# Optimization experiments

Measured on AMD Instinct MI355X. Metric: run time of the kernel, lower is better.

## Reference

```python
import jax, jax.numpy as jnp
import numpy as np

B, C, H, W = 16, 512, 64, 64
CB, CG = 64, 256  # bottleneck = C/8, g = C/2


def _conv1x1(x, w, b):
    # x: [B,Cin,H,W], w: [Cout,Cin] -> [B,Cout,H,W]
    return jnp.einsum('bchw,oc->bohw', x, w) + b[None, :, None, None]


def _avg_pool2(x):
    # 2x2 average pool, stride 2. x: [B,C,H,W] with even H,W.
    b, c, h, w = x.shape
    return x.reshape(b, c, h // 2, 2, w // 2, 2).mean(axis=(3, 5))


def setup_inputs() -> dict:
    key = jax.random.key(0)
    ks = jax.random.split(key, 6)
    s = 0.02
    return {
        'x': jax.random.normal(ks[0], (B, C, H, W), jnp.float32),
        'w_theta': jax.random.normal(ks[1], (CB, C), jnp.float32) * s,
        'b_theta': jnp.zeros((CB,), jnp.float32),
        'w_phi': jax.random.normal(ks[2], (CB, C), jnp.float32) * s,
        'b_phi': jnp.zeros((CB,), jnp.float32),
        'w_g': jax.random.normal(ks[3], (CG, C), jnp.float32) * s,
        'b_g': jnp.zeros((CG,), jnp.float32),
        'w_out': jax.random.normal(ks[4], (C, CG), jnp.float32) * s,
        'b_out': jnp.zeros((C,), jnp.float32),
        'gamma': jnp.zeros((1,), jnp.float32),
    }


def reference(x, w_theta, b_theta, w_phi, b_phi, w_g, b_g, w_out, b_out, gamma):
    b, c, h, w = x.shape
    n = h * w          # query locations
    m = n // 4         # pooled key/value locations

    theta = _conv1x1(x, w_theta, b_theta).reshape(b, CB, n)           # [B,CB,N]
    phi = _avg_pool2(_conv1x1(x, w_phi, b_phi)).reshape(b, CB, m)     # [B,CB,M]
    g = _avg_pool2(_conv1x1(x, w_g, b_g)).reshape(b, CG, m)           # [B,CG,M]

    logits = jnp.einsum('bcn,bcm->bnm', theta, phi)                   # [B,N,M]
    attn = jax.nn.softmax(logits, axis=-1)
    out = jnp.einsum('bcm,bnm->bcn', g, attn).reshape(b, CG, h, w)    # [B,CG,H,W]
    out = _conv1x1(out, w_out, b_out)                                 # [B,C,H,W]
    return gamma[0] * out + x
```

## Files before the change

### kernel.cpp

```cpp
#include <hip/hip_runtime.h>
#include <math.h>


typedef unsigned short u16;
typedef short bf16x8 __attribute__((ext_vector_type(8)));
typedef float f32x16 __attribute__((ext_vector_type(16)));
typedef u16 u16x4 __attribute__((ext_vector_type(4)));
typedef int i32x4 __attribute__((ext_vector_type(4)));

#define MFMA32 __builtin_amdgcn_mfma_f32_32x32x16_bf16
#define B_ 16
#define C_ 512
#define N_ 4096
#define M_ 1024
#define LOG2E 1.44269504088896f
#define FIXMAX 8.0f

__device__ __forceinline__ u16 f2b(float f) {
  unsigned u = __float_as_uint(f);
  return (u16)((u + 0x7FFFu + ((u >> 16) & 1u)) >> 16);
}
__device__ __forceinline__ unsigned cvtpk(float a, float b) {
  unsigned r;
  asm("v_cvt_pk_bf16_f32 %0, %1, %2" : "=v"(r) : "v"(a), "v"(b));
  return r;
}
__device__ __forceinline__ void permswap(unsigned &a, unsigned &b) {
  asm("v_permlane32_swap_b32 %0, %1" : "+v"(a), "+v"(b));
}
__device__ __forceinline__ float exp2v(float a) {
  float r;
  asm("v_exp_f32 %0, %1" : "=v"(r) : "v"(a));
  return r;
}
__device__ __forceinline__ void async_cp16(u16* lds, const u16* g) {
  __builtin_amdgcn_global_load_lds(
      (const __attribute__((address_space(1))) unsigned int*)g,
      (__attribute__((address_space(3))) unsigned int*)lds, 16, 0, 0);
}
__device__ __forceinline__ f32x16 fz16() {
  f32x16 z;
#pragma unroll
  for (int i = 0; i < 16; ++i) z[i] = 0.0f;
  return z;
}


__global__ __launch_bounds__(256) void cvt_all_kernel(
    const float* __restrict__ w_theta, const float* __restrict__ w_phi,
    const float* __restrict__ w_g, const float* __restrict__ w_out,
    const float* __restrict__ gamma, u16* __restrict__ dth, u16* __restrict__ dph,
    u16* __restrict__ dg, u16* __restrict__ dwo) {
  int i = blockIdx.x * 256 + threadIdx.x;
  if (i < 16384) {
    const float* s = (i < 8192) ? w_theta : w_phi;
    u16* d = (i < 8192) ? dth : dph;
    float scale = (i < 8192) ? LOG2E : 1.0f;
    int j = i & 8191;
    int o = j >> 7, c = (j & 127) * 4;
    float4 vv = *(const float4*)(s + (size_t)o * 512 + c);
    int idx = (((o >> 5) * 8 + (c >> 6)) * 4 + ((c >> 4) & 3)) * 512 +
              (((c >> 3) & 1) * 32 + (o & 31)) * 8 + (c & 7);
    u16x4 ot = {f2b(vv.x * scale), f2b(vv.y * scale), f2b(vv.z * scale), f2b(vv.w * scale)};
    *(u16x4*)(d + idx) = ot;
  } else if (i < 49152) {
    int j = i - 16384;
    int o = j >> 7, c = (j & 127) * 4;
    float4 vv = *(const float4*)(w_g + (size_t)o * 512 + c);
    int idx = (((o >> 5) * 8 + (c >> 6)) * 4 + ((c >> 4) & 3)) * 512 +
              (((c >> 3) & 1) * 32 + (o & 31)) * 8 + (c & 7);
    u16x4 ot = {f2b(vv.x), f2b(vv.y), f2b(vv.z), f2b(vv.w)};
    *(u16x4*)(dg + idx) = ot;
  } else {
    int j = i - 49152;
    int o = j >> 6, k = (j & 63) * 4;
    float scale = gamma[0];
    float4 vv = *(const float4*)(w_out + (size_t)o * 256 + k);
    int idx = ((o >> 5) * 16 + (k >> 4)) * 512 +
              (((k >> 3) & 1) * 32 + (o & 31)) * 8 + (k & 7);
    u16x4 ot = {f2b(vv.x * scale), f2b(vv.y * scale), f2b(vv.z * scale), f2b(vv.w * scale)};
    *(u16x4*)(dwo + idx) = ot;
  }
}

__global__ __launch_bounds__(512) void prep_kernel(
    const float* __restrict__ x, const u16* __restrict__ wth,
    const u16* __restrict__ wph, const u16* __restrict__ wg,
    const float* __restrict__ bth, const float* __restrict__ bph,
    const float* __restrict__ bg, u16* __restrict__ th, u16* __restrict__ ph,
    u16* __restrict__ vt) {
  __shared__ u16 xb[128 * 68];
  __shared__ u16 xpt[32 * 68];
  const int t = threadIdx.x;
  const int w = t >> 6, l = t & 63, lo = l & 31, hi = l >> 5;
  const int nb = blockIdx.x, b = blockIdx.y;
  const int n0 = nb * 128;
  const int lcol = (t & 31) * 4;
  const int lrow = t >> 5;

  f32x16 acc0 = fz16(), acc1 = fz16(), a_ph = fz16();

  float v[16];
  auto loadv = [&](int c0) {
#pragma unroll
    for (int i = 0; i < 4; ++i) {
      float4 f = *(const float4*)(x + ((size_t)(b * C_ + c0 + lrow + 16 * i)) * N_ + n0 + lcol);
      v[4*i] = f.x; v[4*i+1] = f.y; v[4*i+2] = f.z; v[4*i+3] = f.w;
    }
  };
  auto writeT = [&]() {
#pragma unroll
    for (int i = 0; i < 4; ++i) {
      int c = lrow + 16 * i;
      int blk = c >> 3;
#pragma unroll
      for (int k = 0; k < 4; ++k) {
        int n = lcol + k;
        int swz = ((n >> 2) ^ (n >> 5)) & 7;
        xb[n * 68 + ((blk ^ swz) * 8) + (c & 7)] = f2b(v[4*i+k]);
      }
    }
    float pA[4], pB[4];
#pragma unroll
    for (int i = 0; i < 4; ++i) {
      pA[i] = v[4*i] + v[4*i+1];
      pB[i] = v[4*i+2] + v[4*i+3];
    }
#pragma unroll
    for (int i = 0; i < 4; ++i) {
      pA[i] += __shfl_xor(pA[i], 16, 64);
      pB[i] += __shfl_xor(pB[i], 16, 64);
    }
    if ((t & 31) < 16) {
      int m0 = (t & 31) * 2;
#pragma unroll
      for (int i = 0; i < 4; ++i) {
        int c = lrow + 16 * i;
        xpt[m0 * 68 + c] = f2b(0.25f * pA[i]);
        xpt[(m0 + 1) * 68 + c] = f2b(0.25f * pB[i]);
      }
    }
  };
  auto domfma = [&](int c0b) {
    if (w < 4) {
      const int n = 32 * w + lo;
      const int rbase = n * 68;
      const int nswz = ((n >> 2) ^ (n >> 5)) & 7;
#pragma unroll
      for (int kh = 0; kh < 4; ++kh) {
        bf16x8 xa = *(const bf16x8*)(&xb[rbase + (((2*kh + hi) ^ nswz) * 8)]);
        bf16x8 w0 = *(const bf16x8*)(wth + ((c0b) * 4 + kh) * 512 + l * 8);
        bf16x8 w1 = *(const bf16x8*)(wth + ((8 + c0b) * 4 + kh) * 512 + l * 8);
        acc0 = MFMA32(xa, w0, acc0, 0, 0, 0);
        acc1 = MFMA32(xa, w1, acc1, 0, 0, 0);
      }
    } else {
      const int wg4 = w - 4;
      const u16* xpw = &xpt[lo * 68];
#pragma unroll
      for (int kh = 0; kh < 4; ++kh) {
        bf16x8 xp8 = *(const bf16x8*)(xpw + kh * 16 + hi * 8);
        bf16x8 g0 = *(const bf16x8*)(wg + ((16*wg4 + c0b) * 4 + kh) * 512 + l * 8);
        bf16x8 g1 = *(const bf16x8*)(wg + ((16*wg4 + 8 + c0b) * 4 + kh) * 512 + l * 8);
        acc0 = MFMA32(g0, xp8, acc0, 0, 0, 0);
        acc1 = MFMA32(g1, xp8, acc1, 0, 0, 0);
        if (wg4 < 2) {
          bf16x8 wp8 = *(const bf16x8*)(wph + ((wg4*8 + c0b) * 4 + kh) * 512 + l * 8);
          a_ph = MFMA32(xp8, wp8, a_ph, 0, 0, 0);
        }
      }
    }
  };

  loadv(0);
  for (int i = 0; i < 8; ++i) {
    if (i) __syncthreads();
    writeT();
    if (i < 7) loadv((i + 1) * 64);
    __syncthreads();
    domfma(i);
  }

  int rr[16];
#pragma unroll
  for (int r = 0; r < 16; ++r) rr[r] = (r & 3) + 8 * (r >> 2) + 4 * hi;

  if (w < 4) {
    u16* thb = th + (size_t)b * 262144;
#pragma unroll
    for (int r = 0; r < 16; ++r) {
      int sub = (((lo >> 3) & 1) * 32 + rr[r]) * 8 + (lo & 7);
      thb[((nb*4 + w)*4 + (lo >> 4)) * 512 + sub]     = f2b(acc0[r] + LOG2E * bth[lo]);
      thb[((nb*4 + w)*4 + 2 + (lo >> 4)) * 512 + sub] = f2b(acc1[r] + LOG2E * bth[32 + lo]);
    }
  } else {
    const int wg4 = w - 4;
    u16* vtb = vt + (size_t)b * 262144;
#pragma unroll
    for (int r = 0; r < 16; ++r) {
      int cg0 = 64 * wg4 + rr[r];
      int sub = (((lo >> 3) & 1) * 32 + rr[r]) * 8 + (lo & 7);
      int kk = (nb & 1) * 2 + (lo >> 4);
      vtb[(((nb >> 1) * 8 + 2*wg4) * 4 + kk) * 512 + sub]     = f2b(acc0[r] + bg[cg0]);
      vtb[(((nb >> 1) * 8 + 2*wg4 + 1) * 4 + kk) * 512 + sub] = f2b(acc1[r] + bg[cg0 + 32]);
    }
    if (wg4 < 2) {
      u16* phb = ph + (size_t)b * 65536;
#pragma unroll
      for (int r = 0; r < 16; ++r) {
        int sub = (((lo >> 3) & 1) * 32 + rr[r]) * 8 + (lo & 7);
        phb[(nb*4 + 2*wg4 + (lo >> 4)) * 512 + sub] = f2b(a_ph[r] + bph[32*wg4 + lo]);
      }
    }
  }
}

__global__ __launch_bounds__(512, 4) void attn_kernel(
    const u16* __restrict__ th, const u16* __restrict__ ph,
    const u16* __restrict__ vt, const u16* __restrict__ wo,
    const float* __restrict__ b_out, const float* __restrict__ gamma,
    const float* __restrict__ x, float* __restrict__ out) {
  __shared__ u16 smem[40960];

  const int t = threadIdx.x;
  const int w = t >> 6, l = t & 63, lo = l & 31, hi = l >> 5;
  const int p = w & 3, h = w >> 2;
  const int flat = blockIdx.y * 32 + blockIdx.x;
  const int nf = (flat & 7) * 64 + (flat >> 3);
  const int b = nf >> 5, nb5 = nf & 31;
  const int qp = nb5 * 128 + 32 * p;

  const u16* thb = th + (size_t)b * 262144;
  const u16* phb = ph + (size_t)b * 65536;
  const u16* vtb = vt + (size_t)b * 262144;

  bf16x8 thB[4];
#pragma unroll
  for (int kh = 0; kh < 4; ++kh)
    thB[kh] = *(const bf16x8*)(thb + ((nb5 * 4 + p) * 4 + kh) * 512 + l * 8);

  f32x16 acc[4];
#pragma unroll
  for (int ct = 0; ct < 4; ++ct) acc[ct] = fz16();
  float sp[4] = {0.0f, 0.0f, 0.0f, 0.0f};

  auto stage = [&](int nbuf, int ic) {
    const int offu = w * 2560;
#pragma unroll
    for (int i = 0; i < 5; ++i) {
      int o = offu + i * 512;
      u16* dst = &smem[nbuf * 20480 + o];
      const u16* src = (o < 16384) ? (vtb + (size_t)ic * 16384 + o + l * 8)
                                   : (phb + (size_t)ic * 4096 + (o - 16384) + l * 8);
      async_cp16(dst, src);
    }
  };

  stage(0, 0);
  asm volatile("s_waitcnt vmcnt(0)" ::: "memory");
  __builtin_amdgcn_sched_barrier(0);
  __builtin_amdgcn_s_barrier();

  int buf = 0;
  for (int ic = 0; ic < 16; ++ic) {
    if (ic < 15) stage(buf ^ 1, ic + 1);

    const u16* Vs = &smem[buf * 20480];
    const u16* Ps = Vs + 16384;
#pragma unroll
    for (int jml = 0; jml < 2; ++jml) {
      bf16x8 pf[4];
#pragma unroll
      for (int kh = 0; kh < 4; ++kh)
        pf[kh] = *(const bf16x8*)(Ps + (jml * 4 + kh) * 512 + l * 8);
      f32x16 S = fz16();
#pragma unroll
      for (int kh = 0; kh < 4; ++kh) S = MFMA32(pf[kh], thB[kh], S, 0, 0, 0);

#pragma unroll
      for (int i = 0; i < 16; ++i) {
        S[i] = exp2v(S[i] - FIXMAX);
        sp[i & 3] += S[i];
      }

      bf16x8 Pf[2];
#pragma unroll
      for (int s = 0; s < 2; ++s) {
        unsigned a0 = cvtpk(S[8*s+0], S[8*s+1]);
        unsigned a1 = cvtpk(S[8*s+2], S[8*s+3]);
        unsigned a2 = cvtpk(S[8*s+4], S[8*s+5]);
        unsigned a3 = cvtpk(S[8*s+6], S[8*s+7]);
        permswap(a0, a2);
        permswap(a1, a3);
        i32x4 wv = {(int)a0, (int)a1, (int)a2, (int)a3};
        Pf[s] = __builtin_bit_cast(bf16x8, wv);
      }

      __builtin_amdgcn_s_setprio(1);
#pragma unroll
      for (int ct2 = 0; ct2 < 4; ++ct2) {
        const u16* vp = Vs + ((4 * h + ct2) * 4 + jml * 2) * 512 + l * 8;
        bf16x8 vf0 = *(const bf16x8*)(vp);
        bf16x8 vf1 = *(const bf16x8*)(vp + 512);
        acc[ct2] = MFMA32(vf0, Pf[0], acc[ct2], 0, 0, 0);
        acc[ct2] = MFMA32(vf1, Pf[1], acc[ct2], 0, 0, 0);
      }
      __builtin_amdgcn_s_setprio(0);
    }

    asm volatile("s_waitcnt vmcnt(0)" ::: "memory");
    __builtin_amdgcn_sched_barrier(0);
    __builtin_amdgcn_s_barrier();
    buf ^= 1;
  }

  float lsum = (sp[0] + sp[1]) + (sp[2] + sp[3]);
  lsum += __shfl_xor(lsum, 32, 64);
  const float linv = 1.0f / lsum;

  __builtin_amdgcn_s_barrier();

  u16* osp = smem + p * 8192;
#pragma unroll
  for (int ct2 = 0; ct2 < 4; ++ct2) {
    f32x16& A = acc[ct2];
#pragma unroll
    for (int s = 0; s < 2; ++s) {
      unsigned a0 = cvtpk(A[8*s+0]*linv, A[8*s+1]*linv);
      unsigned a1 = cvtpk(A[8*s+2]*linv, A[8*s+3]*linv);
      unsigned a2 = cvtpk(A[8*s+4]*linv, A[8*s+5]*linv);
      unsigned a3 = cvtpk(A[8*s+6]*linv, A[8*s+7]*linv);
      permswap(a0, a2);
      permswap(a1, a3);
      i32x4 wv = {(int)a0, (int)a1, (int)a2, (int)a3};
      int f = 8 * h + 2 * ct2 + s;
      int blk8 = 2 * f + hi;
      *(bf16x8*)(osp + lo * 256 + ((blk8 ^ (lo & 7)) * 8)) =
          __builtin_bit_cast(bf16x8, wv);
    }
  }
  __syncthreads();

  bf16x8 Of[16];
#pragma unroll
  for (int f = 0; f < 16; ++f)
    Of[f] = *(const bf16x8*)(osp + lo * 256 + (((2 * f + hi) ^ (lo & 7)) * 8));

  int rr[16];
#pragma unroll
  for (int r = 0; r < 16; ++r) rr[r] = (r & 3) + 8 * (r >> 2) + 4 * hi;

  const float gamma0 = gamma[0];
  for (int ctc = 0; ctc < 8; ++ctc) {
    f32x16 facc = fz16();
    const u16* wp = wo + (size_t)((8 * h + ctc) * 16) * 512 + l * 8;
#pragma unroll
    for (int f = 0; f < 16; ++f) {
      bf16x8 wfr = *(const bf16x8*)(wp + f * 512);
      facc = MFMA32(wfr, Of[f], facc, 0, 0, 0);
    }
#pragma unroll
    for (int r = 0; r < 16; ++r) {
      int c = 256 * h + 32 * ctc + rr[r];
      size_t idx = ((size_t)(b * C_ + c)) * N_ + qp + lo;
      float xv = __builtin_nontemporal_load(&x[idx]);
      __builtin_nontemporal_store(facc[r] + gamma0 * b_out[c] + xv, &out[idx]);
    }
  }
}

extern "C" void kernel_launch(void* const* d_in, const int* in_sizes, int n_in,
                              void* d_out, int out_size, void* d_ws, size_t ws_size,
                              hipStream_t stream) {
  (void)in_sizes; (void)n_in; (void)out_size; (void)ws_size;
  const float* x       = (const float*)d_in[0];
  const float* w_theta = (const float*)d_in[1];
  const float* b_theta = (const float*)d_in[2];
  const float* w_phi   = (const float*)d_in[3];
  const float* b_phi   = (const float*)d_in[4];
  const float* w_g     = (const float*)d_in[5];
  const float* b_g     = (const float*)d_in[6];
  const float* w_out   = (const float*)d_in[7];
  const float* b_out   = (const float*)d_in[8];
  const float* gamma   = (const float*)d_in[9];
  float* out = (float*)d_out;

  char* ws = (char*)d_ws;
  u16* th  = (u16*)(ws);
  u16* ph  = (u16*)(ws + 8388608);
  u16* vt  = (u16*)(ws + 10485760);
  u16* wth = (u16*)(ws + 18874368);
  u16* wph = (u16*)(ws + 18939904);
  u16* wg  = (u16*)(ws + 19005440);
  u16* wo  = (u16*)(ws + 19267584);

  cvt_all_kernel<<<320, 256, 0, stream>>>(w_theta, w_phi, w_g, w_out, gamma,
                                          wth, wph, wg, wo);
  prep_kernel<<<dim3(32, 16), 512, 0, stream>>>(x, wth, wph, wg, b_theta, b_phi,
                                                b_g, th, ph, vt);
  attn_kernel<<<dim3(32, 16), 512, 0, stream>>>(th, ph, vt, wo, b_out, gamma, x, out);
}
```

Measured before the change: 193.8 us.

## Split attention kernel into attention core and separate output-projection kernel

```diff
diff --git a/kernel.cpp b/kernel.cpp
--- a/kernel.cpp
+++ b/kernel.cpp
@@ -215,20 +215,18 @@
   }
 }
 
-__global__ __launch_bounds__(512, 4) void attn_kernel(
+__global__ __launch_bounds__(512, 4) void attn_core_kernel(
     const u16* __restrict__ th, const u16* __restrict__ ph,
-    const u16* __restrict__ vt, const u16* __restrict__ wo,
-    const float* __restrict__ b_out, const float* __restrict__ gamma,
-    const float* __restrict__ x, float* __restrict__ out) {
+    const u16* __restrict__ vt, u16* __restrict__ Og) {
   __shared__ u16 smem[40960];
 
   const int t = threadIdx.x;
-  const int w = t >> 6, l = t & 63, lo = l & 31, hi = l >> 5;
+  const int w = t >> 6, l = t & 63;
   const int p = w & 3, h = w >> 2;
   const int flat = blockIdx.y * 32 + blockIdx.x;
   const int nf = (flat & 7) * 64 + (flat >> 3);
   const int b = nf >> 5, nb5 = nf & 31;
-  const int qp = nb5 * 128 + 32 * p;
+  const int jqt = nb5 * 4 + p;
 
   const u16* thb = th + (size_t)b * 262144;
   const u16* phb = ph + (size_t)b * 65536;
@@ -237,7 +235,7 @@
   bf16x8 thB[4];
 #pragma unroll
   for (int kh = 0; kh < 4; ++kh)
-    thB[kh] = *(const bf16x8*)(thb + ((nb5 * 4 + p) * 4 + kh) * 512 + l * 8);
+    thB[kh] = *(const bf16x8*)(thb + (jqt * 4 + kh) * 512 + l * 8);
 
   f32x16 acc[4];
 #pragma unroll
@@ -308,19 +306,19 @@
       __builtin_amdgcn_s_setprio(0);
     }
 
-    asm volatile("s_waitcnt vmcnt(0)" ::: "memory");
-    __builtin_amdgcn_sched_barrier(0);
-    __builtin_amdgcn_s_barrier();
-    buf ^= 1;
+    if (ic < 15) {
+      asm volatile("s_waitcnt vmcnt(0)" ::: "memory");
+      __builtin_amdgcn_sched_barrier(0);
+      __builtin_amdgcn_s_barrier();
+      buf ^= 1;
+    }
   }
 
   float lsum = (sp[0] + sp[1]) + (sp[2] + sp[3]);
   lsum += __shfl_xor(lsum, 32, 64);
   const float linv = 1.0f / lsum;
 
-  __builtin_amdgcn_s_barrier();
-
-  u16* osp = smem + p * 8192;
+  u16* Ob = Og + (size_t)b * 1048576 + (size_t)jqt * 16 * 512;
 #pragma unroll
   for (int ct2 = 0; ct2 < 4; ++ct2) {
     f32x16& A = acc[ct2];
@@ -334,17 +332,29 @@
       permswap(a1, a3);
       i32x4 wv = {(int)a0, (int)a1, (int)a2, (int)a3};
       int f = 8 * h + 2 * ct2 + s;
-      int blk8 = 2 * f + hi;
-      *(bf16x8*)(osp + lo * 256 + ((blk8 ^ (lo & 7)) * 8)) =
-          __builtin_bit_cast(bf16x8, wv);
-    }
-  }
-  __syncthreads();
-
+      *(bf16x8*)(Ob + f * 512 + l * 8) = __builtin_bit_cast(bf16x8, wv);
+    }
+  }
+}
+
+__global__ __launch_bounds__(512, 4) void outconv_kernel(
+    const u16* __restrict__ Og, const u16* __restrict__ wo,
+    const float* __restrict__ b_out, const float* __restrict__ gamma,
+    const float* __restrict__ x, float* __restrict__ out) {
+  const int t = threadIdx.x;
+  const int w = t >> 6, l = t & 63, lo = l & 31, hi = l >> 5;
+  const int p = w & 3, h = w >> 2;
+  const int flat = blockIdx.y * 32 + blockIdx.x;
+  const int nf = (flat & 7) * 64 + (flat >> 3);
+  const int b = nf >> 5, nb5 = nf & 31;
+  const int jqt = nb5 * 4 + p;
+  const int qp = jqt * 32;
+
+  const u16* Ob = Og + (size_t)b * 1048576 + (size_t)jqt * 16 * 512;
   bf16x8 Of[16];
 #pragma unroll
   for (int f = 0; f < 16; ++f)
-    Of[f] = *(const bf16x8*)(osp + lo * 256 + (((2 * f + hi) ^ (lo & 7)) * 8));
+    Of[f] = *(const bf16x8*)(Ob + f * 512 + l * 8);
 
   int rr[16];
 #pragma unroll
@@ -393,10 +403,12 @@
   u16* wph = (u16*)(ws + 18939904);
   u16* wg  = (u16*)(ws + 19005440);
   u16* wo  = (u16*)(ws + 19267584);
+  u16* Og  = (u16*)(ws + 19529728);
 
   cvt_all_kernel<<<320, 256, 0, stream>>>(w_theta, w_phi, w_g, w_out, gamma,
                                           wth, wph, wg, wo);
   prep_kernel<<<dim3(32, 16), 512, 0, stream>>>(x, wth, wph, wg, b_theta, b_phi,
                                                 b_g, th, ph, vt);
-  attn_kernel<<<dim3(32, 16), 512, 0, stream>>>(th, ph, vt, wo, b_out, gamma, x, out);
-}
+  attn_core_kernel<<<dim3(32, 16), 512, 0, stream>>>(th, ph, vt, Og);
+  outconv_kernel<<<dim3(32, 16), 512, 0, stream>>>(Og, wo, b_out, gamma, x, out);
+}
```

Result: faster. 172.4 us (-11.1%).
